# Kernel tuning notes

Measured on AMD Instinct MI355X. Metric: run time of the kernel, lower is better.

Reference implementation:

```python
import jax, jax.numpy as jnp
import numpy as np

N_NODES = 50000
N_EDGES = 800000
D_IN = 128
HIDDEN = 128
N_GRAPHS = 256
N_CLASSES = 10
NEG_SLOPE = 0.2


def gatv2_conv(x, src, dst, Wl, Wr, att, bias, num_nodes):
    # PyG GATv2Conv, heads=1, add_self_loops handled by caller via src/dst.
    xl = x @ Wl  # [N, H] source transform
    xr = x @ Wr  # [N, H] target transform
    # per-edge attention logits: a^T LeakyReLU(xl[src] + xr[dst])
    e = jax.nn.leaky_relu(xl[src] + xr[dst], NEG_SLOPE) @ att  # [E]
    # segment softmax over incoming edges of each dst node
    e_max = jax.ops.segment_max(e, dst, num_segments=num_nodes)
    e_exp = jnp.exp(e - e_max[dst])
    denom = jax.ops.segment_sum(e_exp, dst, num_segments=num_nodes)
    alpha = e_exp / (denom[dst] + 1e-16)  # [E]
    out = jax.ops.segment_sum(alpha[:, None] * xl[src], dst, num_segments=num_nodes)
    return out + bias


def setup_inputs() -> dict:
    key = jax.random.key(0)
    ks = jax.random.split(key, 12)
    x = jax.random.normal(ks[0], (N_NODES, D_IN), dtype=jnp.float32)
    edge_index = jax.random.randint(ks[1], (2, N_EDGES), 0, N_NODES, dtype=jnp.int64)
    batch = jnp.sort(jax.random.randint(ks[2], (N_NODES,), 0, N_GRAPHS, dtype=jnp.int64))
    s = 1.0 / np.sqrt(D_IN)
    sh = 1.0 / np.sqrt(HIDDEN)
    return {
        "x": x, "edge_index": edge_index, "batch": batch,
        "Wl1": jax.random.normal(ks[3], (D_IN, HIDDEN), jnp.float32) * s,
        "Wr1": jax.random.normal(ks[4], (D_IN, HIDDEN), jnp.float32) * s,
        "att1": jax.random.normal(ks[5], (HIDDEN,), jnp.float32) * sh,
        "b1": jnp.zeros((HIDDEN,), jnp.float32),
        "g_ln": jnp.ones((HIDDEN,), jnp.float32),
        "b_ln": jnp.zeros((HIDDEN,), jnp.float32),
        "Wl2": jax.random.normal(ks[6], (HIDDEN, HIDDEN), jnp.float32) * sh,
        "Wr2": jax.random.normal(ks[7], (HIDDEN, HIDDEN), jnp.float32) * sh,
        "att2": jax.random.normal(ks[8], (HIDDEN,), jnp.float32) * sh,
        "b2": jnp.zeros((HIDDEN,), jnp.float32),
        "Wlin": jax.random.normal(ks[9], (HIDDEN, N_CLASSES), jnp.float32) * sh,
        "blin": jnp.zeros((N_CLASSES,), jnp.float32),
    }


def reference(x, edge_index, batch, Wl1, Wr1, att1, b1, g_ln, b_ln,
              Wl2, Wr2, att2, b2, Wlin, blin):
    n = x.shape[0]
    # add self loops (PyG GATv2Conv default add_self_loops=True)
    loops = jnp.arange(n, dtype=edge_index.dtype)
    src = jnp.concatenate([edge_index[0], loops])
    dst = jnp.concatenate([edge_index[1], loops])

    h = gatv2_conv(x, src, dst, Wl1, Wr1, att1, b1, n)
    h = jax.nn.relu(h)
    # layer norm over feature dim
    mu = jnp.mean(h, axis=-1, keepdims=True)
    var = jnp.var(h, axis=-1, keepdims=True)
    h = (h - mu) * jax.lax.rsqrt(var + 1e-5) * g_ln + b_ln

    h = gatv2_conv(h, src, dst, Wl2, Wr2, att2, b2, n)

    # global mean pool per graph
    sums = jax.ops.segment_sum(h, batch, num_segments=N_GRAPHS)
    cnts = jax.ops.segment_sum(jnp.ones((n,), h.dtype), batch, num_segments=N_GRAPHS)
    pooled = sums / jnp.maximum(cnts, 1.0)[:, None]
    # dropout p=0.4 is identity in eval mode
    return pooled @ Wlin + blin
```

## Files before the change

### kernel.cpp

```cpp
#include <hip/hip_runtime.h>
#include <hip/hip_bf16.h>
#include <hip/hip_fp16.h>

#define NN 50000
#define NE 800000
#define HID 128
#define NG 256
#define NC 10
#define NB 196
#define CHUNK 4096
#define BCAP 8192
#define SCB 196
#define MGB 782

using half8  = __attribute__((ext_vector_type(8))) _Float16;
using half2v = __attribute__((ext_vector_type(2))) _Float16;
using f32x4  = __attribute__((ext_vector_type(4))) float;

__device__ __forceinline__ float fdot2f(unsigned a, unsigned b, float c)
{
#if __has_builtin(__builtin_amdgcn_fdot2)
    return __builtin_amdgcn_fdot2(*(half2v*)&a, *(half2v*)&b, c, false);
#else
    float2 fa = __half22float2(*(__half2*)&a);
    float2 fb = __half22float2(*(__half2*)&b);
    return fmaf(fa.x, fb.x, fmaf(fa.y, fb.y, c));
#endif
}

__device__ __forceinline__ unsigned addleaky_h2(unsigned xl, unsigned xr)
{
    half2v s = *(half2v*)&xl + *(half2v*)&xr;
    half2v l = __builtin_elementwise_max(s, s * (_Float16)0.2f);
    return *(unsigned*)&l;
}

__global__ __launch_bounds__(256) void k_wpackz(
    const float* __restrict__ Wl1, const float* __restrict__ Wr1,
    const float* __restrict__ Wl2, const float* __restrict__ Wr2,
    __half* __restrict__ wpk1, __half* __restrict__ wpk2,
    int* __restrict__ cursor)
{
    int gidx = blockIdx.x * 256 + threadIdx.x;
    if (gidx < 256) cursor[gidx] = 0;

    int idx = gidx & 4095;
    int layer = gidx >> 12;
    const float* Wl = layer ? Wl2 : Wl1;
    const float* Wr = layer ? Wr2 : Wr1;
    __half* wpk = layer ? wpk2 : wpk1;

    int t = idx >> 8;
    int lane = idx & 63;
    const float* W = (t < 8) ? Wl : Wr;
    int col = ((t & 7) << 4) + (lane & 15);
    int k0 = (((idx >> 6) & 3) << 5) + ((lane >> 4) << 3);
    __half tmp[8];
#pragma unroll
    for (int j = 0; j < 8; j++)
        tmp[j] = __float2half(W[(size_t)(k0 + j) * 128 + col]);
    *(uint4*)(wpk + ((size_t)idx << 3)) = *(uint4*)tmp;
}

template <bool F32IN>
__device__ __forceinline__ void mgemm_body(
    int blk, const void* __restrict__ in, const __half* __restrict__ wpk,
    __half* __restrict__ xlh, __half* __restrict__ xrh)
{
    const int w = threadIdx.x >> 6;
    const int lane = threadIdx.x & 63;
    const int nodebase = blk * 64 + w * 16;
    const int lrow = lane & 15;
    const int kb = lane >> 4;

    const int nload = min(nodebase + lrow, NN - 1);

    half8 a[4];
    if constexpr (F32IN) {
        const float* xp = (const float*)in + (size_t)nload * 128 + (kb << 3);
#pragma unroll
        for (int kf = 0; kf < 4; kf++) {
            float4 f0 = *(const float4*)(xp + kf * 32);
            float4 f1 = *(const float4*)(xp + kf * 32 + 4);
            half8 hh;
            hh[0] = (_Float16)f0.x; hh[1] = (_Float16)f0.y;
            hh[2] = (_Float16)f0.z; hh[3] = (_Float16)f0.w;
            hh[4] = (_Float16)f1.x; hh[5] = (_Float16)f1.y;
            hh[6] = (_Float16)f1.z; hh[7] = (_Float16)f1.w;
            a[kf] = hh;
        }
    } else {
        const char* xp = (const char*)in + (size_t)nload * 256 + (kb << 4);
#pragma unroll
        for (int kf = 0; kf < 4; kf++) {
            uint4 u = *(const uint4*)(xp + kf * 64);
            a[kf] = *(half8*)&u;
        }
    }

    const uint4* wp = (const uint4*)wpk + lane;

#pragma unroll
    for (int t = 0; t < 16; t++) {
        f32x4 acc = {0.f, 0.f, 0.f, 0.f};
#pragma unroll
        for (int kf = 0; kf < 4; kf++) {
            uint4 bu = wp[(t * 4 + kf) * 64];
            half8 b = *(half8*)&bu;
            acc = __builtin_amdgcn_mfma_f32_16x16x32_f16(a[kf], b, acc, 0, 0, 0);
        }
        int col = ((t & 7) << 4) + lrow;
#pragma unroll
        for (int i = 0; i < 4; i++) {
            int node = nodebase + kb * 4 + i;
            if (node < NN) {
                if (t < 8) xlh[(size_t)node * 128 + col] = __float2half(acc[i]);
                else       xrh[(size_t)node * 128 + col] = __float2half(acc[i]);
            }
        }
    }
}

__device__ __forceinline__ int block_scan_incl(int v, int t)
{
    __shared__ int sm[256];
    sm[t] = v;
    __syncthreads();
#pragma unroll
    for (int off = 1; off < 256; off <<= 1) {
        int u = (t >= off) ? sm[t - off] : 0;
        __syncthreads();
        sm[t] += u;
        __syncthreads();
    }
    return sm[t];
}

__device__ __forceinline__ void bscatter_body(
    int blk, const int* __restrict__ ei, int* __restrict__ cursor,
    unsigned* __restrict__ pairbuf)
{
    __shared__ int lcnt[256], cstart[256], lcur[256], gpos[256];
    __shared__ unsigned sorted[CHUNK];
    __shared__ unsigned char sortedB[CHUNK];
    const int t = threadIdx.x;
    const int base = blk * CHUNK;
    const int n = min(CHUNK, NE - base);
    if (n <= 0) return;

    lcnt[t] = 0;
    __syncthreads();

    unsigned pk[16];
    int bk[16];
#pragma unroll
    for (int i = 0; i < 16; i++) {
        int off = i * 256 + t;
        bk[i] = -1;
        if (off < n) {
            int e = base + off;
            int s = ei[e], d = ei[NE + e];
            bk[i] = d >> 8;
            pk[i] = ((unsigned)s << 8) | (unsigned)(d & 255);
            atomicAdd(&lcnt[bk[i]], 1);
        }
    }
    __syncthreads();

    int v = lcnt[t];
    int inc = block_scan_incl(v, t);
    cstart[t] = inc - v;
    lcur[t] = inc - v;
    __syncthreads();
    gpos[t] = (v > 0) ? atomicAdd(&cursor[t], v) : 0;
    __syncthreads();

#pragma unroll
    for (int i = 0; i < 16; i++) {
        if (bk[i] >= 0) {
            int r = atomicAdd(&lcur[bk[i]], 1);
            sorted[r] = pk[i];
            sortedB[r] = (unsigned char)bk[i];
        }
    }
    __syncthreads();

    for (int j = t; j < n; j += 256) {
        int b = sortedB[j];
        pairbuf[(size_t)b * BCAP + gpos[b] + (j - cstart[b])] = sorted[j];
    }
}

__global__ __launch_bounds__(256) void k_bscmg(
    const int* __restrict__ ei, int* __restrict__ cursor,
    unsigned* __restrict__ pairbuf, const float* __restrict__ x,
    const __half* __restrict__ wpk1, __half* __restrict__ xlh,
    __half* __restrict__ xrh)
{
    if (blockIdx.x < SCB)
        bscatter_body(blockIdx.x, ei, cursor, pairbuf);
    else
        mgemm_body<true>(blockIdx.x - SCB, x, wpk1, xlh, xrh);
}

__global__ __launch_bounds__(256) void k_mgemm2(
    const __half* __restrict__ in, const __half* __restrict__ wpk,
    __half* __restrict__ xlh, __half* __restrict__ xrh)
{
    mgemm_body<false>(blockIdx.x, in, wpk, xlh, xrh);
}

__global__ __launch_bounds__(256) void k_bbuild(
    const unsigned* __restrict__ pairbuf, const int* __restrict__ cursor,
    int* __restrict__ rowptr, int* __restrict__ esrc)
{
    __shared__ int pre[256];
    __shared__ int ncnt[256], cur[256];
    const int b = blockIdx.x;
    const int t = threadIdx.x;
    const int node0 = b * 256;
    const int nnodes = min(256, NN - node0);

    int cb = (t < NB) ? cursor[t] : 0;
    int nodes = (t < NB) ? min(256, NN - t * 256) : 0;
    int inc = block_scan_incl(cb + nodes, t);
    pre[t] = inc;
    __syncthreads();
    const int row0 = (b == 0) ? 0 : pre[b - 1];
    const int cnt = cursor[b];
    const unsigned* pb = pairbuf + (size_t)b * BCAP;

    ncnt[t] = 0;
    __syncthreads();
    for (int i = t; i < cnt; i += 256)
        atomicAdd(&ncnt[pb[i] & 255u], 1);
    __syncthreads();

    int v = (t < nnodes) ? ncnt[t] + 1 : 0;
    int inc2 = block_scan_incl(v, t);
    int rb = row0 + inc2 - v;
    if (t < nnodes) {
        rowptr[node0 + t] = rb;
        esrc[rb] = node0 + t;
        cur[t] = rb + 1;
    }
    if (b == NB - 1 && t == 0) rowptr[NN] = NE + NN;
    __syncthreads();

    for (int i = t; i < cnt; i += 256) {
        unsigned p = pb[i];
        int pos = atomicAdd(&cur[p & 255u], 1);
        esrc[pos] = (int)(p >> 8);
    }
}

#define GAT_LOGIT(A, e)                                                     \
    {                                                                       \
        unsigned l0 = addleaky_h2(A.x, xrq.x);                              \
        unsigned l1 = addleaky_h2(A.y, xrq.y);                              \
        unsigned l2 = addleaky_h2(A.z, xrq.z);                              \
        unsigned l3 = addleaky_h2(A.w, xrq.w);                              \
        e = fdot2f(l0, atq.x, 0.f);                                         \
        e = fdot2f(l1, atq.y, e);                                           \
        e = fdot2f(l2, atq.z, e);                                           \
        e = fdot2f(l3, atq.w, e);                                           \
        _Pragma("unroll")                                                   \
        for (int off = 8; off; off >>= 1) e += __shfl_xor(e, off, 64);      \
    }

#define GAT_ACC(A, p)                                                       \
    {                                                                       \
        half8 ah = *(half8*)&A;                                             \
        _Pragma("unroll")                                                   \
        for (int i = 0; i < 8; i++)                                         \
            acc[i] = fmaf(p, (float)ah[i], acc[i]);                         \
    }

__device__ __forceinline__ void gat_core(
    const char* __restrict__ xlb, const int* __restrict__ esrc,
    int beg, int end, int lane, const uint4 xrq, const uint4 atq,
    float* acc, float& den)
{
    const int g = lane >> 4;
    const unsigned qb = (unsigned)((lane & 15) << 4);
#pragma unroll
    for (int i = 0; i < 8; i++) acc[i] = 0.f;
    den = 0.f;

    for (int sc = beg; sc < end; sc += 64) {
        const int nv = min(end - sc, 64);
        const int nit = (nv + 3) >> 2;
        const int nfull = nv >> 2;
        int myidx = esrc[sc + lane] & 0xFFFF;

        auto LD = [&](int j) -> uint4 {
            int t = (j << 2) + g;
            int s = __shfl(myidx, t, 64);
            unsigned off = ((unsigned)s << 8) | qb;
            return *(const uint4*)(xlb + off);
        };

        uint4 A = LD(0);
        uint4 B = LD(1 < nit ? 1 : 0);

#pragma unroll 2
        for (int jj = 0; jj < nfull; ++jj) {
            uint4 C = LD(jj + 2 < nit ? jj + 2 : nit - 1);
            float e;
            GAT_LOGIT(A, e)
            float p = __expf(fminf(e, 80.f));
            den += p;
            GAT_ACC(A, p)
            A = B; B = C;
        }
        if (nv & 3) {
            float e;
            GAT_LOGIT(A, e)
            float p = ((nfull << 2) + g < nv) ? __expf(fminf(e, 80.f)) : 0.f;
            den += p;
            GAT_ACC(A, p)
        }
    }

#pragma unroll
    for (int off = 16; off < 64; off <<= 1) {
        den += __shfl_xor(den, off, 64);
#pragma unroll
        for (int i = 0; i < 8; i++) acc[i] += __shfl_xor(acc[i], off, 64);
    }
}

__device__ __forceinline__ uint4 ld_att_h2(const float* att, int q)
{
    float4 c = *(const float4*)(att + q * 8);
    float4 e = *(const float4*)(att + q * 8 + 4);
    __half2 t0 = __floats2half2_rn(c.x, c.y);
    __half2 t1 = __floats2half2_rn(c.z, c.w);
    __half2 t2 = __floats2half2_rn(e.x, e.y);
    __half2 t3 = __floats2half2_rn(e.z, e.w);
    uint4 r;
    r.x = *(unsigned*)&t0; r.y = *(unsigned*)&t1;
    r.z = *(unsigned*)&t2; r.w = *(unsigned*)&t3;
    return r;
}

__global__ __launch_bounds__(256, 8) void k_gat1(
    const char* __restrict__ xlb, const char* __restrict__ xrb,
    const float* __restrict__ att, const int* __restrict__ rowptr,
    const int* __restrict__ esrc, const float* __restrict__ bias,
    const float* __restrict__ g_ln, const float* __restrict__ b_ln,
    char* __restrict__ h16b)
{
    int d = (int)((blockIdx.x * 256 + threadIdx.x) >> 6);
    int lane = threadIdx.x & 63;
    int q = lane & 15;

    uint4 xrq = *(const uint4*)(xrb + ((size_t)d << 8) + (q << 4));
    uint4 atq = ld_att_h2(att, q);

    float acc[8]; float den;
    gat_core(xlb, esrc, rowptr[d], rowptr[d + 1], lane, xrq, atq, acc, den);

    float inv = 1.f / (den + 1e-16f);
    float x[8];
    {
        float4 a = *(const float4*)(bias + q * 8);
        float4 b = *(const float4*)(bias + q * 8 + 4);
        float bb[8] = {a.x,a.y,a.z,a.w,b.x,b.y,b.z,b.w};
#pragma unroll
        for (int i = 0; i < 8; i++) x[i] = fmaxf(fmaf(acc[i], inv, bb[i]), 0.f);
    }

    float s1 = 0.f, s2 = 0.f;
#pragma unroll
    for (int i = 0; i < 8; i++) { s1 += x[i]; s2 += x[i] * x[i]; }
#pragma unroll
    for (int off = 8; off; off >>= 1) {
        s1 += __shfl_xor(s1, off, 64);
        s2 += __shfl_xor(s2, off, 64);
    }
    float mu = s1 * (1.f / 128.f);
    float var = s2 * (1.f / 128.f) - mu * mu;
    float rstd = rsqrtf(var + 1e-5f);

    if (lane < 16) {
        float4 ga = *(const float4*)(g_ln + q * 8);
        float4 gb = *(const float4*)(g_ln + q * 8 + 4);
        float4 ba = *(const float4*)(b_ln + q * 8);
        float4 bb = *(const float4*)(b_ln + q * 8 + 4);
        float o[8];
        o[0] = (x[0]-mu)*rstd*ga.x + ba.x;
        o[1] = (x[1]-mu)*rstd*ga.y + ba.y;
        o[2] = (x[2]-mu)*rstd*ga.z + ba.z;
        o[3] = (x[3]-mu)*rstd*ga.w + ba.w;
        o[4] = (x[4]-mu)*rstd*gb.x + bb.x;
        o[5] = (x[5]-mu)*rstd*gb.y + bb.y;
        o[6] = (x[6]-mu)*rstd*gb.z + bb.z;
        o[7] = (x[7]-mu)*rstd*gb.w + bb.w;
        __half2 p0 = __floats2half2_rn(o[0], o[1]);
        __half2 p1 = __floats2half2_rn(o[2], o[3]);
        __half2 p2 = __floats2half2_rn(o[4], o[5]);
        __half2 p3 = __floats2half2_rn(o[6], o[7]);
        uint4 u;
        u.x = *(unsigned*)&p0; u.y = *(unsigned*)&p1;
        u.z = *(unsigned*)&p2; u.w = *(unsigned*)&p3;
        *(uint4*)(h16b + ((size_t)d << 8) + (q << 4)) = u;
    }
}

__global__ __launch_bounds__(256, 8) void k_gat2(
    const char* __restrict__ xlb, const char* __restrict__ xrb,
    const float* __restrict__ att, const int* __restrict__ rowptr,
    const int* __restrict__ esrc, const float* __restrict__ bias,
    char* __restrict__ h2b)
{
    int d = (int)((blockIdx.x * 256 + threadIdx.x) >> 6);
    int lane = threadIdx.x & 63;
    int q = lane & 15;

    uint4 xrq = *(const uint4*)(xrb + ((size_t)d << 8) + (q << 4));
    uint4 atq = ld_att_h2(att, q);

    float acc[8]; float den;
    gat_core(xlb, esrc, rowptr[d], rowptr[d + 1], lane, xrq, atq, acc, den);

    float inv = 1.f / (den + 1e-16f);
    if (lane < 16) {
        float4 a = *(const float4*)(bias + q * 8);
        float4 b = *(const float4*)(bias + q * 8 + 4);
        float o[8];
        o[0] = fmaf(acc[0], inv, a.x);
        o[1] = fmaf(acc[1], inv, a.y);
        o[2] = fmaf(acc[2], inv, a.z);
        o[3] = fmaf(acc[3], inv, a.w);
        o[4] = fmaf(acc[4], inv, b.x);
        o[5] = fmaf(acc[5], inv, b.y);
        o[6] = fmaf(acc[6], inv, b.z);
        o[7] = fmaf(acc[7], inv, b.w);
        __half2 p0 = __floats2half2_rn(o[0], o[1]);
        __half2 p1 = __floats2half2_rn(o[2], o[3]);
        __half2 p2 = __floats2half2_rn(o[4], o[5]);
        __half2 p3 = __floats2half2_rn(o[6], o[7]);
        uint4 u;
        u.x = *(unsigned*)&p0; u.y = *(unsigned*)&p1;
        u.z = *(unsigned*)&p2; u.w = *(unsigned*)&p3;
        *(uint4*)(h2b + ((size_t)d << 8) + (q << 4)) = u;
    }
}

__global__ __launch_bounds__(128) void k_poolin(
    const __half* __restrict__ h2h, const int* __restrict__ batch,
    const float* __restrict__ W, const float* __restrict__ b,
    float* __restrict__ out)
{
    const int g = blockIdx.x;
    const int f = threadIdx.x;

    int lo = 0, hi = NN;
    while (lo < hi) { int m = (lo + hi) >> 1; if (batch[m] < g) lo = m + 1; else hi = m; }
    int lo2 = lo, hi2 = NN;
    while (lo2 < hi2) { int m = (lo2 + hi2) >> 1; if (batch[m] <= g) lo2 = m + 1; else hi2 = m; }

    float s = 0.f;
    const int last = lo2 - 1;
    for (int n = lo; n < lo2; n += 8) {
        float v[8];
#pragma unroll
        for (int j = 0; j < 8; j++) {
            int nn = min(n + j, last);
            v[j] = __half2float(h2h[(size_t)nn * 128 + f]);
        }
#pragma unroll
        for (int j = 0; j < 8; j++)
            s += (n + j < lo2) ? v[j] : 0.f;
    }

    __shared__ float sm[128];
    sm[f] = s;
    __syncthreads();

    if (f < NC) {
        float invc = 1.f / fmaxf((float)(lo2 - lo), 1.f);
        float a = 0.f;
        for (int k = 0; k < HID; k++)
            a = fmaf(sm[k], W[(size_t)k * NC + f], a);
        out[(size_t)g * NC + f] = fmaf(a, invc, b[f]);
    }
}

extern "C" void kernel_launch(void* const* d_in, const int* in_sizes, int n_in,
                              void* d_out, int out_size, void* d_ws, size_t ws_size,
                              hipStream_t stream)
{
    const float* x     = (const float*)d_in[0];
    const int*   ei    = (const int*)d_in[1];
    const int*   batch = (const int*)d_in[2];
    const float* Wl1   = (const float*)d_in[3];
    const float* Wr1   = (const float*)d_in[4];
    const float* att1  = (const float*)d_in[5];
    const float* b1    = (const float*)d_in[6];
    const float* g_ln  = (const float*)d_in[7];
    const float* b_ln  = (const float*)d_in[8];
    const float* Wl2   = (const float*)d_in[9];
    const float* Wr2   = (const float*)d_in[10];
    const float* att2  = (const float*)d_in[11];
    const float* b2    = (const float*)d_in[12];
    const float* Wlin  = (const float*)d_in[13];
    const float* blin  = (const float*)d_in[14];
    float* out = (float*)d_out;

    char* ws = (char*)d_ws;
    __half* xlh16 = (__half*)ws;
    char*   xlb   = ws;
    __half* xrh16 = (__half*)(ws + (size_t)NN * 256);
    char*   xrb   = (char*)xrh16;
    __half* h16   = xrh16 + (size_t)NN * 128;
    __half* h2h   = h16 + (size_t)NN * 128;
    char*   h2b   = (char*)h2h;
    int* rowptr   = (int*)(h2h + (size_t)NN * 128);
    int* esrc     = rowptr + NN + 1;
    unsigned* pairbuf = (unsigned*)(esrc + NE + NN);
    int* cursor   = (int*)(pairbuf + (size_t)NB * BCAP);
    __half* wpk1  = (__half*)(cursor + 256);
    __half* wpk2  = wpk1 + 32768;

    const int gat_blocks = (NN * 64) / 256;

    k_wpackz<<<32, 256, 0, stream>>>(Wl1, Wr1, Wl2, Wr2, wpk1, wpk2, cursor);

    k_bscmg<<<SCB + MGB, 256, 0, stream>>>(ei, cursor, pairbuf, x, wpk1,
                                           xlh16, xrh16);

    k_bbuild<<<NB, 256, 0, stream>>>(pairbuf, cursor, rowptr, esrc);

    k_gat1<<<gat_blocks, 256, 0, stream>>>(xlb, xrb, att1, rowptr, esrc,
                                           b1, g_ln, b_ln, (char*)h16);

    k_mgemm2<<<MGB, 256, 0, stream>>>(h16, wpk2, xlh16, xrh16);

    k_gat2<<<gat_blocks, 256, 0, stream>>>(xlb, xrb, att2, rowptr, esrc,
                                           b2, h2b);

    k_poolin<<<NG, 128, 0, stream>>>(h2h, batch, Wlin, blin, out);
}
```

Measured before the change: 154.7 us.

## Regroup preprocessing kernels to overlap weight packing with scatter and CSR build with GEMM

The three setup kernels are regrouped into two. Weight packing now shares a launch with the edge bucket-scatter, and the CSR build shares a launch with the first-layer feature GEMM. This respects the real dependencies (the GEMM needs the packed weights, the CSR build needs the scatter output) while removing one kernel launch and letting independent work run concurrently. The cursor is now zeroed with a memset, which adds an async memset node in exchange.

New measurement: 156.9 us. No clear change (+1.4%).

```diff
diff --git a/kernel.cpp b/kernel.cpp
--- a/kernel.cpp
+++ b/kernel.cpp
@@ -12,6 +12,7 @@
 #define BCAP 8192
 #define SCB 196
 #define MGB 782
+#define WPB 32
 
 using half8  = __attribute__((ext_vector_type(8))) _Float16;
 using half2v = __attribute__((ext_vector_type(2))) _Float16;
@@ -35,15 +36,12 @@
     return *(unsigned*)&l;
 }
 
-__global__ __launch_bounds__(256) void k_wpackz(
-    const float* __restrict__ Wl1, const float* __restrict__ Wr1,
+__device__ __forceinline__ void wpack_body(
+    int blk, const float* __restrict__ Wl1, const float* __restrict__ Wr1,
     const float* __restrict__ Wl2, const float* __restrict__ Wr2,
-    __half* __restrict__ wpk1, __half* __restrict__ wpk2,
-    int* __restrict__ cursor)
-{
-    int gidx = blockIdx.x * 256 + threadIdx.x;
-    if (gidx < 256) cursor[gidx] = 0;
-
+    __half* __restrict__ wpk1, __half* __restrict__ wpk2)
+{
+    int gidx = blk * 256 + threadIdx.x;
     int idx = gidx & 4095;
     int layer = gidx >> 12;
     const float* Wl = layer ? Wl2 : Wl1;
@@ -191,32 +189,12 @@
     }
 }
 
-__global__ __launch_bounds__(256) void k_bscmg(
-    const int* __restrict__ ei, int* __restrict__ cursor,
-    unsigned* __restrict__ pairbuf, const float* __restrict__ x,
-    const __half* __restrict__ wpk1, __half* __restrict__ xlh,
-    __half* __restrict__ xrh)
-{
-    if (blockIdx.x < SCB)
-        bscatter_body(blockIdx.x, ei, cursor, pairbuf);
-    else
-        mgemm_body<true>(blockIdx.x - SCB, x, wpk1, xlh, xrh);
-}
-
-__global__ __launch_bounds__(256) void k_mgemm2(
-    const __half* __restrict__ in, const __half* __restrict__ wpk,
-    __half* __restrict__ xlh, __half* __restrict__ xrh)
-{
-    mgemm_body<false>(blockIdx.x, in, wpk, xlh, xrh);
-}
-
-__global__ __launch_bounds__(256) void k_bbuild(
-    const unsigned* __restrict__ pairbuf, const int* __restrict__ cursor,
+__device__ __forceinline__ void bbuild_body(
+    int b, const unsigned* __restrict__ pairbuf, const int* __restrict__ cursor,
     int* __restrict__ rowptr, int* __restrict__ esrc)
 {
     __shared__ int pre[256];
     __shared__ int ncnt[256], cur[256];
-    const int b = blockIdx.x;
     const int t = threadIdx.x;
     const int node0 = b * 256;
     const int nnodes = min(256, NN - node0);
@@ -252,6 +230,38 @@
         int pos = atomicAdd(&cur[p & 255u], 1);
         esrc[pos] = (int)(p >> 8);
     }
+}
+
+__global__ __launch_bounds__(256) void k_wpsc(
+    const float* __restrict__ Wl1, const float* __restrict__ Wr1,
+    const float* __restrict__ Wl2, const float* __restrict__ Wr2,
+    __half* __restrict__ wpk1, __half* __restrict__ wpk2,
+    const int* __restrict__ ei, int* __restrict__ cursor,
+    unsigned* __restrict__ pairbuf)
+{
+    if (blockIdx.x < WPB)
+        wpack_body(blockIdx.x, Wl1, Wr1, Wl2, Wr2, wpk1, wpk2);
+    else
+        bscatter_body(blockIdx.x - WPB, ei, cursor, pairbuf);
+}
+
+__global__ __launch_bounds__(256) void k_bdmg(
+    const unsigned* __restrict__ pairbuf, const int* __restrict__ cursor,
+    int* __restrict__ rowptr, int* __restrict__ esrc,
+    const float* __restrict__ x, const __half* __restrict__ wpk1,
+    __half* __restrict__ xlh, __half* __restrict__ xrh)
+{
+    if (blockIdx.x < NB)
+        bbuild_body(blockIdx.x, pairbuf, cursor, rowptr, esrc);
+    else
+        mgemm_body<true>(blockIdx.x - NB, x, wpk1, xlh, xrh);
+}
+
+__global__ __launch_bounds__(256) void k_mgemm2(
+    const __half* __restrict__ in, const __half* __restrict__ wpk,
+    __half* __restrict__ xlh, __half* __restrict__ xrh)
+{
+    mgemm_body<false>(blockIdx.x, in, wpk, xlh, xrh);
 }
 
 #define GAT_LOGIT(A, e)                                                     \
@@ -526,12 +536,13 @@
 
     const int gat_blocks = (NN * 64) / 256;
 
-    k_wpackz<<<32, 256, 0, stream>>>(Wl1, Wr1, Wl2, Wr2, wpk1, wpk2, cursor);
-
-    k_bscmg<<<SCB + MGB, 256, 0, stream>>>(ei, cursor, pairbuf, x, wpk1,
-                                           xlh16, xrh16);
-
-    k_bbuild<<<NB, 256, 0, stream>>>(pairbuf, cursor, rowptr, esrc);
+    hipMemsetAsync(cursor, 0, 256 * sizeof(int), stream);
+
+    k_wpsc<<<WPB + SCB, 256, 0, stream>>>(Wl1, Wr1, Wl2, Wr2, wpk1, wpk2,
+                                          ei, cursor, pairbuf);
+
+    k_bdmg<<<NB + MGB, 256, 0, stream>>>(pairbuf, cursor, rowptr, esrc,
+                                         x, wpk1, xlh16, xrh16);
 
     k_gat1<<<gat_blocks, 256, 0, stream>>>(xlb, xrb, att1, rowptr, esrc,
                                            b1, g_ln, b_ln, (char*)h16);
```
